# Kernel tuning notes

Measured on AMD Instinct MI355X. Metric: run time of the kernel, lower is better.

The kernel has to match this reference:

```python
import jax, jax.numpy as jnp
import numpy as np

B = 64          # graphs per batch
NN = 4096       # nodes per graph (64x64 lattice)
N = B * NN      # total nodes
DEG = 4         # avg degree
E = N * DEG     # total directed edges
DIN, H, L = 1, 128, 64


def setup_inputs() -> dict:
    key = jax.random.key(0)
    ks = jax.random.split(key, 16)
    x = jax.random.normal(ks[0], (N, DIN), dtype=jnp.float32)
    eps = jax.random.normal(ks[1], (B, L), dtype=jnp.float32)
    # per-graph random edges, offset so they never cross graphs
    src = jax.random.randint(ks[2], (E,), 0, NN)
    dst = jax.random.randint(ks[3], (E,), 0, NN)
    off = (jnp.arange(E) // (NN * DEG)) * NN
    edge_index = jnp.stack([src + off, dst + off]).astype(jnp.int32)
    batch = (jnp.arange(N) // NN).astype(jnp.int32)
    s = 0.02
    p = lambda k, shp: s * jax.random.normal(k, shp, dtype=jnp.float32)
    return {
        "x": x, "eps": eps,
        "enc_w1": p(ks[4], (DIN, H)), "enc_b1": jnp.zeros((H,), jnp.float32),
        "enc_w2": p(ks[5], (H, H)),   "enc_b2": jnp.zeros((H,), jnp.float32),
        "mu_w": p(ks[6], (H, L)),     "mu_b": jnp.zeros((L,), jnp.float32),
        "lv_w": p(ks[7], (H, L)),     "lv_b": jnp.zeros((L,), jnp.float32),
        "zn_w": p(ks[8], (L, H)),     "zn_b": jnp.zeros((H,), jnp.float32),
        "dec_w1": p(ks[9], (H, H)),   "dec_b1": jnp.zeros((H,), jnp.float32),
        "dec_w2": p(ks[10], (H, H)),  "dec_b2": jnp.zeros((H,), jnp.float32),
        "out_w": p(ks[11], (H, 1)),   "out_b": jnp.zeros((1,), jnp.float32),
        "edge_index": edge_index, "batch": batch,
    }


def _gcn(h, w, b, row, col, norm, n):
    # PyG GCNConv: xW -> gather at row, scale by sym-norm, scatter-sum at col, + bias
    hw = h @ w
    msg = hw[row] * norm[:, None]
    return jax.ops.segment_sum(msg, col, num_segments=n) + b


def reference(x, eps, enc_w1, enc_b1, enc_w2, enc_b2, mu_w, mu_b, lv_w, lv_b,
              zn_w, zn_b, dec_w1, dec_b1, dec_w2, dec_b2, out_w, out_b,
              edge_index, batch):
    n = x.shape[0]
    b = eps.shape[0]
    nn_ = n // b
    # add self-loops, symmetric GCN normalization (shared by all convs)
    loops = jnp.arange(n, dtype=edge_index.dtype)
    row = jnp.concatenate([edge_index[0], loops])
    col = jnp.concatenate([edge_index[1], loops])
    deg = jax.ops.segment_sum(jnp.ones_like(col, dtype=x.dtype), col, num_segments=n)
    dinv = jnp.where(deg > 0, jax.lax.rsqrt(deg), 0.0)
    norm = dinv[row] * dinv[col]
    h = jax.nn.relu(_gcn(x, enc_w1, enc_b1, row, col, norm, n))
    h = jax.nn.relu(_gcn(h, enc_w2, enc_b2, row, col, norm, n))
    cnt = jax.ops.segment_sum(jnp.ones((n,), x.dtype), batch, num_segments=b)
    hg = jax.ops.segment_sum(h, batch, num_segments=b) / cnt[:, None]
    mu = hg @ mu_w + mu_b
    logvar = hg @ lv_w + lv_b
    # ---- reparameterize ----
    z = mu + jnp.exp(0.5 * logvar) * eps
    zn = z @ zn_w + zn_b          # [B, H]
    hd = zn[batch]                # [N, H]
    hd = jax.nn.relu(_gcn(hd, dec_w1, dec_b1, row, col, norm, n))
    hd = jax.nn.relu(_gcn(hd, dec_w2, dec_b2, row, col, norm, n))
    spin = jnp.tanh(hd @ out_w + out_b)   # [N, 1]
    recon = spin.reshape(b, nn_)
    return (recon, mu, logvar, z)
```

## Files before the change

kernel.cpp:

```cpp
#include <hip/hip_runtime.h>
#include <math.h>

#define NTOT 262144
#define BG   64
#define NNPG 4096
#define ET   1048576
#define EPG  16384
#define EPB  4096
#define HD   128
#define LD   64
#define NSEG 129
#define TN   256
#define MCAP ET

__device__ __forceinline__ void swz(int b, int& g, int& j){
  int xcd = b & 7, q = b >> 3;
  g = (q >> 2)*8 + xcd;
  j = q & 3;
}

__device__ __forceinline__ void tab_base(
    int tid, const float* __restrict__ wsrc, const float* __restrict__ bsrc,
    const float* __restrict__ w2, float* __restrict__ tout, int* __restrict__ nfout,
    float* __restrict__ ACg,
    float* ws, float* bs, int* ks, float (*red)[128][4], int* nfsh)
{
  int k = tid & 127, qg = tid >> 7;
  if (qg == 0){
    float w = wsrc[k], b = bsrc[k];
    float t; int kind;
    if (w != 0.0f){ t = -b / w; kind = (w > 0.0f) ? 0 : 1; }
    else          { t = INFINITY; kind = 2; }
    ws[k] = w; bs[k] = b; ks[k] = kind;
    if (tout) tout[k] = t;
  }
  __syncthreads();
  if (tid == 0){
    int c = 0;
    for (int q = 0; q < 128; q++) c += (ks[q] != 2) ? 1 : 0;
    *nfsh = c;
    if (nfout) *nfout = c;
  }
  float a0=0.f, c0=0.f, an=0.f, cn=0.f;
  #pragma unroll
  for (int u = 0; u < 16; u++){
    int q = qg*16 + u;
    float v = w2[q*HD + k];
    int kd = ks[q];
    float wq = ws[q], bq = bs[q];
    bool m0 = (kd == 1) || (kd == 2 && bq > 0.f);
    bool mn = (kd == 0) || (kd == 2 && bq > 0.f);
    float wv = wq*v, bv = bq*v;
    a0 += m0 ? wv : 0.f; c0 += m0 ? bv : 0.f;
    an += mn ? wv : 0.f; cn += mn ? bv : 0.f;
  }
  red[qg][k][0]=a0; red[qg][k][1]=c0; red[qg][k][2]=an; red[qg][k][3]=cn;
  __syncthreads();
  int nf = *nfsh;
  int base = (k>>2)*8 + (k&3);
  if (qg == 0){
    float A0=0.f,C0=0.f,An=0.f,Cn=0.f;
    #pragma unroll
    for (int p = 0; p < 8; p++){
      A0+=red[p][k][0]; C0+=red[p][k][1]; An+=red[p][k][2]; Cn+=red[p][k][3];
    }
    ACg[base] = A0; ACg[base+4] = C0;
    ACg[(size_t)nf*256 + base] = An; ACg[(size_t)nf*256 + base + 4] = Cn;
  }
}

__device__ __forceinline__ void tab_extras(
    int g, int tid, const float* __restrict__ wsrc, const float* __restrict__ bsrc,
    const float* __restrict__ w2, const int* __restrict__ segUsed,
    const int* __restrict__ nfA, float* __restrict__ ACbase,
    float* ws, float* bs, float* tsh, int* ks, int* rr, float (*red)[128][4])
{
  int nf = nfA[g];
  unsigned any = 0;
  for (int wd = 0; wd < 5; wd++){
    unsigned m = (unsigned)segUsed[g*8 + wd];
    if (wd == 0) m &= ~1u;
    if ((nf >> 5) == wd) m &= ~(1u << (nf & 31));
    any |= m;
  }
  if (any == 0) return;
  int k = tid & 127, qg = tid >> 7;
  if (qg == 0){
    float w = wsrc[g*HD + k], b = bsrc[k];
    float t; int kind;
    if (w != 0.0f){ t = -b / w; kind = (w > 0.0f) ? 0 : 1; }
    else          { t = INFINITY; kind = 2; }
    ws[k] = w; bs[k] = b; tsh[k] = t; ks[k] = kind;
  }
  __syncthreads();
  if (qg == 0){
    float t = tsh[k];
    int r = 0;
    for (int q = 0; q < 128; q++){
      if (ks[q] != 2){
        float tq = tsh[q];
        if (tq < t || (tq == t && q < k)) r++;
      }
    }
    rr[k] = r;
  }
  __syncthreads();
  float* ACg = ACbase + (size_t)g*NSEG*256;
  int base = (k>>2)*8 + (k&3);
  for (int wd = 0; wd < 5; wd++){
    unsigned m = (unsigned)segUsed[g*8 + wd];
    if (wd == 0) m &= ~1u;
    if ((nf >> 5) == wd) m &= ~(1u << (nf & 31));
    while (m){
      int bit = __ffs(m) - 1;
      m &= m - 1;
      int s = wd*32 + bit;
      float pa=0.f, pc=0.f;
      #pragma unroll
      for (int u = 0; u < 16; u++){
        int q = qg*16 + u;
        int kd = ks[q];
        bool act = (kd == 0) ? (rr[q] < s) : (kd == 1) ? (rr[q] >= s) : (bs[q] > 0.f);
        float v = act ? w2[q*HD + k] : 0.f;
        pa = fmaf(ws[q], v, pa); pc = fmaf(bs[q], v, pc);
      }
      red[qg][k][0]=pa; red[qg][k][1]=pc;
      __syncthreads();
      if (qg == 0){
        float A=0.f,C=0.f;
        #pragma unroll
        for (int p = 0; p < 8; p++){ A+=red[p][k][0]; C+=red[p][k][1]; }
        ACg[(size_t)s*256 + base] = A; ACg[(size_t)s*256 + base + 4] = C;
      }
      __syncthreads();
    }
  }
}

__global__ void __launch_bounds__(1024) k_count(const int* __restrict__ ei,
                                                const float* __restrict__ w1,
                                                const float* __restrict__ b1,
                                                const float* __restrict__ w2,
                                                int* __restrict__ cntJ,
                                                float* __restrict__ t1, int* __restrict__ nfp,
                                                float* __restrict__ AC1,
                                                float* __restrict__ hgsum,
                                                int* __restrict__ mcnt,
                                                int* __restrict__ segU1,
                                                int* __restrict__ segU){
  __shared__ union {
    int h[NNPG];
    struct { float ws[128], bs[128]; int ks[128], nfsh;
             float red[8][128][4]; } t;
  } u;
  int tid = threadIdx.x;
  if (blockIdx.x == 256){
    for (int idx = tid; idx < BG*HD; idx += 1024) hgsum[idx] = 0.f;
    if (tid < 2) mcnt[tid] = 0;
    if (tid < 8) segU1[tid] = 0;
    if (tid < BG*8) segU[tid] = 0;
    tab_base(tid, w1, b1, w2, t1, nfp, AC1,
             u.t.ws, u.t.bs, u.t.ks, u.t.red, &u.t.nfsh);
    return;
  }
  int g, j; swz(blockIdx.x, g, j);
  #pragma unroll
  for (int k = tid; k < NNPG; k += 1024) u.h[k] = 0;
  __syncthreads();
  int gbase = g*NNPG;
  const int4* dsts4 = (const int4*)(ei + ET + g*EPG + j*EPB);
  int4 D = dsts4[tid];
  atomicAdd(&u.h[D.x - gbase], 1); atomicAdd(&u.h[D.y - gbase], 1);
  atomicAdd(&u.h[D.z - gbase], 1); atomicAdd(&u.h[D.w - gbase], 1);
  __syncthreads();
  int* plane = cntJ + j*NTOT + gbase;
  #pragma unroll
  for (int k = tid; k < NNPG; k += 1024) plane[k] = u.h[k];
}

__global__ void __launch_bounds__(1024) k_edge1(
    const int* __restrict__ ei, const int* __restrict__ cntJ,
    const float* __restrict__ x, float2* __restrict__ xd,
    float2* __restrict__ accJ)
{
  __shared__ float2 sxd[NNPG];
  __shared__ float ax[NNPG];
  __shared__ float s1[NNPG];
  int tid = threadIdx.x;
  int g, j; swz(blockIdx.x, g, j);
  int gbase = g*NNPG;
  const int4* srcs4 = (const int4*)(ei + g*EPG + j*EPB);
  const int4* dsts4 = (const int4*)(ei + ET + g*EPG + j*EPB);
  int4 S = srcs4[tid], D = dsts4[tid];
  {
    int i0 = 4*tid;
    int4 c0 = *(const int4*)(cntJ + 0*NTOT + gbase + i0);
    int4 c1 = *(const int4*)(cntJ + 1*NTOT + gbase + i0);
    int4 c2 = *(const int4*)(cntJ + 2*NTOT + gbase + i0);
    int4 c3 = *(const int4*)(cntJ + 3*NTOT + gbase + i0);
    float4 xv = *(const float4*)(x + gbase + i0);
    float2 p0 = make_float2(xv.x, rsqrtf((float)(c0.x+c1.x+c2.x+c3.x) + 1.0f));
    float2 p1 = make_float2(xv.y, rsqrtf((float)(c0.y+c1.y+c2.y+c3.y) + 1.0f));
    float2 p2 = make_float2(xv.z, rsqrtf((float)(c0.z+c1.z+c2.z+c3.z) + 1.0f));
    float2 p3 = make_float2(xv.w, rsqrtf((float)(c0.w+c1.w+c2.w+c3.w) + 1.0f));
    sxd[i0+0] = p0; sxd[i0+1] = p1; sxd[i0+2] = p2; sxd[i0+3] = p3;
    if (j == 0){
      float4* xd4 = (float4*)(xd + gbase);
      xd4[2*tid+0] = make_float4(p0.x, p0.y, p1.x, p1.y);
      xd4[2*tid+1] = make_float4(p2.x, p2.y, p3.x, p3.y);
    }
    *(float4*)(ax + i0) = make_float4(0.f,0.f,0.f,0.f);
    *(float4*)(s1 + i0) = make_float4(0.f,0.f,0.f,0.f);
  }
  __syncthreads();
  #define P1(s_, d_) { float2 sd = sxd[(s_) - gbase]; int dl = (d_) - gbase; \
    atomicAdd(&ax[dl], sd.y * sd.x); \
    atomicAdd(&s1[dl], sd.y); }
  P1(S.x, D.x); P1(S.y, D.y); P1(S.z, D.z); P1(S.w, D.w);
  #undef P1
  __syncthreads();
  float4* ap = (float4*)(accJ + (size_t)j*NTOT + gbase);
  ap[2*tid+0] = make_float4(ax[4*tid+0], s1[4*tid+0], ax[4*tid+1], s1[4*tid+1]);
  ap[2*tid+1] = make_float4(ax[4*tid+2], s1[4*tid+2], ax[4*tid+3], s1[4*tid+3]);
}

__global__ void k_pack(const float2* __restrict__ xd, const float2* __restrict__ accJ,
                       const float* __restrict__ t1,
                       float4* __restrict__ rec, float* __restrict__ srowA,
                       int* __restrict__ segU1){
  __shared__ float ts[128];
  __shared__ int used[8];
  int tid = threadIdx.x;
  if (tid < 128) ts[tid] = t1[tid];
  if (tid < 8) used[tid] = 0;
  __syncthreads();
  int i = blockIdx.x*256 + tid;
  float2 xdv = xd[i];
  float2 a0 = accJ[0*NTOT + i], a1 = accJ[1*NTOT + i];
  float2 a2 = accJ[2*NTOT + i], a3 = accJ[3*NTOT + i];
  float axs = (a0.x + a1.x) + (a2.x + a3.x);
  float s1s = (a0.y + a1.y) + (a2.y + a3.y);
  float di = xdv.y;
  float ax = di * (di * xdv.x + axs);
  float sr = di * (di + s1s);
  int sc = 0;
  for (int q = 0; q < 128; q++) sc += (ts[q] < ax) ? 1 : 0;
  rec[i] = make_float4(di, di*ax, di*sr, __int_as_float(sc));
  srowA[i] = sr;
  atomicOr(&used[sc>>5], 1u << (sc & 31));
  __syncthreads();
  if (tid < 8 && used[tid]) atomicOr(&segU1[tid], used[tid]);
}

__global__ void __launch_bounds__(1024) k_edge2enc(
    const int* __restrict__ ei, const float4* __restrict__ rec,
    const int* __restrict__ nfp, float4* __restrict__ sums4,
    int2* __restrict__ missL, int* __restrict__ mcnt,
    const float* __restrict__ enc_w1, const float* __restrict__ enc_b1,
    const float* __restrict__ enc_w2, const int* __restrict__ segU1,
    float* __restrict__ AC1)
{
  __shared__ union {
    float sf[NNPG*4];
    struct { float ws[128], bs[128], tsh[128];
             int ks[128], rr[128]; float red[8][128][4]; } t;
  } u;
  int tid = threadIdx.x;
  if (blockIdx.x == 256){
    tab_extras(0, tid, enc_w1, enc_b1, enc_w2, segU1, nfp, AC1,
               u.t.ws, u.t.bs, u.t.tsh, u.t.ks, u.t.rr, u.t.red);
    return;
  }
  int g, j; swz(blockIdx.x, g, j);
  int gbase = g*NNPG;
  int nf = nfp[0];
  const int4* srcs4 = (const int4*)(ei + g*EPG + j*EPB);
  const int4* dsts4 = (const int4*)(ei + ET + g*EPG + j*EPB);
  int4 S = srcs4[tid], D = dsts4[tid];
  float4 r1 = rec[S.x], r2 = rec[S.y], r3 = rec[S.z], r4 = rec[S.w];
  float4* sf4 = (float4*)u.sf;
  #pragma unroll
  for (int k = 0; k < 4; k++) sf4[tid + k*1024] = make_float4(0.f,0.f,0.f,0.f);
  __syncthreads();
  #define E1(r_, s_, d_) { int dl = (d_) - gbase; int sb = __float_as_int(r_.w); \
    atomicAdd(&u.sf[dl*4+0], r_.y); atomicAdd(&u.sf[dl*4+1], r_.x); \
    if (sb == nf) { atomicAdd(&u.sf[dl*4+2], r_.y); atomicAdd(&u.sf[dl*4+3], r_.x); } \
    else if (sb != 0) { int ix = atomicAdd(&mcnt[0], 1); \
      if (ix < MCAP) missL[ix] = make_int2(d_, s_); } }
  E1(r1, S.x, D.x); E1(r2, S.y, D.y); E1(r3, S.z, D.z); E1(r4, S.w, D.w);
  #undef E1
  __syncthreads();
  float4* sp = sums4 + (size_t)j*NTOT + gbase;
  #pragma unroll
  for (int k = 0; k < 4; k++) sp[tid + k*1024] = sf4[tid + k*1024];
}

__global__ void __launch_bounds__(256) k_enc_fin(
    const float4* __restrict__ rec, const float4* __restrict__ sums4,
    const float4* __restrict__ AC, const float* __restrict__ b2,
    const int* __restrict__ nfp, const int2* __restrict__ missL,
    const int* __restrict__ mcnt, float* __restrict__ hgsum)
{
  __shared__ float4 sS[TN];
  __shared__ float4 sRA[TN];
  __shared__ float red[256*4];
  int bid = blockIdx.x, g = bid & 63, part = bid >> 6;
  int tid = threadIdx.x, lane = tid & 31, nrow = tid >> 5;
  int base = g*NNPG + part*TN;
  int nf = nfp[0];
  {
    int i = base + tid;
    sRA[tid] = rec[i];
    float4 a = sums4[0*NTOT + i], b = sums4[1*NTOT + i];
    float4 c = sums4[2*NTOT + i], d = sums4[3*NTOT + i];
    sS[tid] = make_float4(a.x+b.x+c.x+d.x, a.y+b.y+c.y+d.y,
                          a.z+b.z+c.z+d.z, a.w+b.w+c.w+d.w);
  }
  __syncthreads();
  const float4* q0 = AC + (size_t)lane*2;
  const float4* qn = AC + ((size_t)nf*32 + lane)*2;
  float4 A0 = q0[0], C0 = q0[1], An = qn[0], Cn = qn[1];
  float4 dA = make_float4(An.x-A0.x, An.y-A0.y, An.z-A0.z, An.w-A0.w);
  float4 dC = make_float4(Cn.x-C0.x, Cn.y-C0.y, Cn.z-C0.z, Cn.w-C0.w);
  float4 bb = ((const float4*)b2)[lane];
  int mc = mcnt[0]; mc = mc < MCAP ? mc : MCAP;
  float gx=0.f, gy=0.f, gz=0.f, gw=0.f;
  for (int it = 0; it < TN/8; ++it){
    int li = it*8 + nrow;
    int i = base + li;
    float4 rA = sRA[li];
    float4 s4 = sS[li];
    float accx = fmaf(s4.x,A0.x, fmaf(s4.z,dA.x, fmaf(s4.y,C0.x, s4.w*dC.x)));
    float accy = fmaf(s4.x,A0.y, fmaf(s4.z,dA.y, fmaf(s4.y,C0.y, s4.w*dC.y)));
    float accz = fmaf(s4.x,A0.z, fmaf(s4.z,dA.z, fmaf(s4.y,C0.z, s4.w*dC.z)));
    float accw = fmaf(s4.x,A0.w, fmaf(s4.z,dA.w, fmaf(s4.y,C0.w, s4.w*dC.w)));
    if (mc > 0){
      for (int e = 0; e < mc; e++){
        int2 me = missL[e];
        if (me.x == i){
          float4 r = rec[me.y];
          int sb = __float_as_int(r.w);
          const float4* qm = AC + ((size_t)sb*32 + lane)*2;
          float4 qa = qm[0], qc = qm[1];
          accx = fmaf(r.y, qa.x-A0.x, fmaf(r.x, qc.x-C0.x, accx));
          accy = fmaf(r.y, qa.y-A0.y, fmaf(r.x, qc.y-C0.y, accy));
          accz = fmaf(r.y, qa.z-A0.z, fmaf(r.x, qc.z-C0.z, accz));
          accw = fmaf(r.y, qa.w-A0.w, fmaf(r.x, qc.w-C0.w, accw));
        }
      }
    }
    int si = __float_as_int(rA.w);
    bool m0 = (si == 0);
    float4 sa, sc;
    sa.x = m0 ? A0.x : An.x; sa.y = m0 ? A0.y : An.y; sa.z = m0 ? A0.z : An.z; sa.w = m0 ? A0.w : An.w;
    sc.x = m0 ? C0.x : Cn.x; sc.y = m0 ? C0.y : Cn.y; sc.z = m0 ? C0.z : Cn.z; sc.w = m0 ? C0.w : Cn.w;
    if (si != 0 && si != nf){
      const float4* qs = AC + ((size_t)si*32 + lane)*2;
      sa = qs[0]; sc = qs[1];
    }
    float d = rA.x, d2 = d*d, ca = rA.y*d;
    gx += fmaxf(fmaf(d, accx, fmaf(ca, sa.x, d2*sc.x)) + bb.x, 0.f);
    gy += fmaxf(fmaf(d, accy, fmaf(ca, sa.y, d2*sc.y)) + bb.y, 0.f);
    gz += fmaxf(fmaf(d, accz, fmaf(ca, sa.z, d2*sc.z)) + bb.z, 0.f);
    gw += fmaxf(fmaf(d, accw, fmaf(ca, sa.w, d2*sc.w)) + bb.w, 0.f);
  }
  __syncthreads();
  red[tid*4+0] = gx; red[tid*4+1] = gy; red[tid*4+2] = gz; red[tid*4+3] = gw;
  __syncthreads();
  if (nrow == 0){
    float tx=0.f, ty=0.f, tz=0.f, tw=0.f;
    for (int r2 = 0; r2 < 8; r2++){
      int t2 = (r2*32 + lane)*4;
      tx += red[t2]; ty += red[t2+1]; tz += red[t2+2]; tw += red[t2+3];
    }
    atomicAdd(&hgsum[g*HD + lane*4 + 0], tx);
    atomicAdd(&hgsum[g*HD + lane*4 + 1], ty);
    atomicAdd(&hgsum[g*HD + lane*4 + 2], tz);
    atomicAdd(&hgsum[g*HD + lane*4 + 3], tw);
  }
}

__global__ void __launch_bounds__(1024) k_small(
    const float* __restrict__ hgsum,
    const float* __restrict__ mu_w, const float* __restrict__ mu_b,
    const float* __restrict__ lv_w, const float* __restrict__ lv_b,
    const float* __restrict__ eps,
    const float* __restrict__ zn_w, const float* __restrict__ zn_b,
    const float* __restrict__ dec_w1, const float* __restrict__ dec_b1,
    const float* __restrict__ dec_w2,
    float* __restrict__ out_mu, float* __restrict__ out_lv, float* __restrict__ out_z,
    float* __restrict__ t2, float* __restrict__ ushG, int* __restrict__ nf2,
    float* __restrict__ AC2)
{
  __shared__ float hg[128], zsh[64], znsh[128], ush[128], bsx[128];
  __shared__ int ks[128], nfsh;
  __shared__ float red[8][128][4];
  int g = blockIdx.x, tid = threadIdx.x;
  if (tid < 128) hg[tid] = hgsum[g*HD + tid] * (1.0f/4096.0f);
  __syncthreads();
  if (tid < 64){
    int l = tid;
    float m = mu_b[l], v = lv_b[l];
    for (int k = 0; k < HD; k++){
      float hv = hg[k];
      m = fmaf(hv, mu_w[k*LD + l], m);
      v = fmaf(hv, lv_w[k*LD + l], v);
    }
    int o = g*LD + l;
    out_mu[o] = m; out_lv[o] = v;
    float zv = fmaf(expf(0.5f*v), eps[o], m);
    out_z[o] = zv; zsh[l] = zv;
  }
  __syncthreads();
  if (tid < 128){
    float acc = zn_b[tid];
    for (int l = 0; l < LD; l++) acc = fmaf(zsh[l], zn_w[l*HD + tid], acc);
    znsh[tid] = acc;
  }
  __syncthreads();
  if (tid < 128){
    float acc = 0.f;
    for (int j = 0; j < HD; j++) acc = fmaf(znsh[j], dec_w1[j*HD + tid], acc);
    ushG[g*HD + tid] = acc;
    ush[tid] = acc;
    float b = dec_b1[tid];
    bsx[tid] = b;
    float t; int kind;
    if (acc != 0.0f){ t = -b / acc; kind = (acc > 0.0f) ? 0 : 1; }
    else            { t = INFINITY; kind = 2; }
    t2[g*HD + tid] = t; ks[tid] = kind;
  }
  __syncthreads();
  if (tid == 0){
    int c = 0;
    for (int q = 0; q < 128; q++) c += (ks[q] != 2) ? 1 : 0;
    nf2[g] = c; nfsh = c;
  }
  __syncthreads();
  int k = tid & 127, qg = tid >> 7;
  float a0=0.f, c0=0.f, an=0.f, cn=0.f;
  #pragma unroll
  for (int u = 0; u < 16; u++){
    int q = qg*16 + u;
    float v = dec_w2[q*HD + k];
    int kd = ks[q];
    float wq = ush[q], bq = bsx[q];
    bool m0 = (kd == 1) || (kd == 2 && bq > 0.f);
    bool mn = (kd == 0) || (kd == 2 && bq > 0.f);
    float wv = wq*v, bv = bq*v;
    a0 += m0 ? wv : 0.f; c0 += m0 ? bv : 0.f;
    an += mn ? wv : 0.f; cn += mn ? bv : 0.f;
  }
  red[qg][k][0]=a0; red[qg][k][1]=c0; red[qg][k][2]=an; red[qg][k][3]=cn;
  __syncthreads();
  if (qg == 0){
    float A0=0.f,C0=0.f,An=0.f,Cn=0.f;
    #pragma unroll
    for (int p = 0; p < 8; p++){
      A0+=red[p][k][0]; C0+=red[p][k][1]; An+=red[p][k][2]; Cn+=red[p][k][3];
    }
    float* ACg = AC2 + (size_t)g*NSEG*256;
    int base = (k>>2)*8 + (k&3);
    int nf = nfsh;
    ACg[base] = A0; ACg[base+4] = C0;
    ACg[(size_t)nf*256 + base] = An; ACg[(size_t)nf*256 + base + 4] = Cn;
  }
}

__global__ void k_seg2(const float* __restrict__ t2, const float* __restrict__ srowA,
                       float4* __restrict__ rec, int* __restrict__ segUsed){
  __shared__ float ts[128];
  __shared__ int used[8];
  int tid = threadIdx.x;
  int i = blockIdx.x*256 + tid;
  int g = blockIdx.x >> 4;
  if (tid < 128) ts[tid] = t2[g*HD + tid];
  if (tid < 8) used[tid] = 0;
  __syncthreads();
  float a = srowA[i];
  int sc = 0;
  for (int q = 0; q < 128; q++) sc += (ts[q] < a) ? 1 : 0;
  float4 r = rec[i];
  r.y = __int_as_float(sc);
  rec[i] = r;
  atomicOr(&used[sc>>5], 1u << (sc & 31));
  __syncthreads();
  if (tid < 8 && used[tid]) atomicOr(&segUsed[g*8 + tid], used[tid]);
}

__global__ void __launch_bounds__(1024) k_edge2dec(
    const int* __restrict__ ei, const float4* __restrict__ rec,
    const int* __restrict__ nf2, float4* __restrict__ sums4,
    int2* __restrict__ missL, int* __restrict__ mcnt,
    const float* __restrict__ ushG, const float* __restrict__ dec_b1,
    const float* __restrict__ dec_w2, const int* __restrict__ segU,
    float* __restrict__ AC2)
{
  __shared__ union {
    float sf[NNPG*4];
    struct { float ws[128], bs[128], tsh[128];
             int ks[128], rr[128]; float red[8][128][4]; } t;
  } u;
  int tid = threadIdx.x;
  if (blockIdx.x >= 256){
    tab_extras(blockIdx.x - 256, tid, ushG, dec_b1, dec_w2, segU, nf2, AC2,
               u.t.ws, u.t.bs, u.t.tsh, u.t.ks, u.t.rr, u.t.red);
    return;
  }
  int g, j; swz(blockIdx.x, g, j);
  int gbase = g*NNPG;
  int nf = nf2[g];
  const int4* srcs4 = (const int4*)(ei + g*EPG + j*EPB);
  const int4* dsts4 = (const int4*)(ei + ET + g*EPG + j*EPB);
  int4 S = srcs4[tid], D = dsts4[tid];
  float4 r1 = rec[S.x], r2 = rec[S.y], r3 = rec[S.z], r4 = rec[S.w];
  float4* sf4 = (float4*)u.sf;
  #pragma unroll
  for (int k = 0; k < 4; k++) sf4[tid + k*1024] = make_float4(0.f,0.f,0.f,0.f);
  __syncthreads();
  #define E2(r_, s_, d_) { int dl = (d_) - gbase; int sb = __float_as_int(r_.y); \
    atomicAdd(&u.sf[dl*4+0], r_.z); atomicAdd(&u.sf[dl*4+1], r_.x); \
    if (sb == nf) { atomicAdd(&u.sf[dl*4+2], r_.z); atomicAdd(&u.sf[dl*4+3], r_.x); } \
    else if (sb != 0) { int ix = atomicAdd(&mcnt[1], 1); \
      if (ix < MCAP) missL[ix] = make_int2(d_, s_); } }
  E2(r1, S.x, D.x); E2(r2, S.y, D.y); E2(r3, S.z, D.z); E2(r4, S.w, D.w);
  #undef E2
  __syncthreads();
  float4* sp = sums4 + (size_t)j*NTOT + gbase;
  #pragma unroll
  for (int k = 0; k < 4; k++) sp[tid + k*1024] = sf4[tid + k*1024];
}

__global__ void __launch_bounds__(256) k_dec_fin(
    const float4* __restrict__ rec, const float4* __restrict__ sums4,
    const float4* __restrict__ AC2, const float* __restrict__ b2,
    const float* __restrict__ ow, const float* __restrict__ ob,
    const int* __restrict__ nf2, const int2* __restrict__ missL,
    const int* __restrict__ mcnt, float* __restrict__ recon)
{
  __shared__ float4 sS[TN];
  __shared__ float4 sRA[TN];
  int bid = blockIdx.x, g = bid & 63, part = bid >> 6;
  int tid = threadIdx.x, lane = tid & 31, nrow = tid >> 5;
  int base = g*NNPG + part*TN;
  int nf = nf2[g];
  const float4* AC = AC2 + (size_t)g*NSEG*64;
  {
    int i = base + tid;
    sRA[tid] = rec[i];
    float4 a = sums4[0*NTOT + i], b = sums4[1*NTOT + i];
    float4 c = sums4[2*NTOT + i], d = sums4[3*NTOT + i];
    sS[tid] = make_float4(a.x+b.x+c.x+d.x, a.y+b.y+c.y+d.y,
                          a.z+b.z+c.z+d.z, a.w+b.w+c.w+d.w);
  }
  __syncthreads();
  const float4* q0 = AC + (size_t)lane*2;
  const float4* qn = AC + ((size_t)nf*32 + lane)*2;
  float4 A0 = q0[0], C0 = q0[1], An = qn[0], Cn = qn[1];
  float4 dA = make_float4(An.x-A0.x, An.y-A0.y, An.z-A0.z, An.w-A0.w);
  float4 dC = make_float4(Cn.x-C0.x, Cn.y-C0.y, Cn.z-C0.z, Cn.w-C0.w);
  float4 bb  = ((const float4*)b2)[lane];
  float4 owv = ((const float4*)ow)[lane];
  float obv = ob[0];
  int mc = mcnt[1]; mc = mc < MCAP ? mc : MCAP;
  for (int it = 0; it < TN/8; ++it){
    int li = it*8 + nrow;
    int i = base + li;
    float4 rA = sRA[li];
    float4 s4 = sS[li];
    float accx = fmaf(s4.x,A0.x, fmaf(s4.z,dA.x, fmaf(s4.y,C0.x, s4.w*dC.x)));
    float accy = fmaf(s4.x,A0.y, fmaf(s4.z,dA.y, fmaf(s4.y,C0.y, s4.w*dC.y)));
    float accz = fmaf(s4.x,A0.z, fmaf(s4.z,dA.z, fmaf(s4.y,C0.z, s4.w*dC.z)));
    float accw = fmaf(s4.x,A0.w, fmaf(s4.z,dA.w, fmaf(s4.y,C0.w, s4.w*dC.w)));
    if (mc > 0){
      for (int e = 0; e < mc; e++){
        int2 me = missL[e];
        if (me.x == i){
          float4 r = rec[me.y];
          int sb = __float_as_int(r.y);
          const float4* qm = AC + ((size_t)sb*32 + lane)*2;
          float4 qa = qm[0], qc = qm[1];
          accx = fmaf(r.z, qa.x-A0.x, fmaf(r.x, qc.x-C0.x, accx));
          accy = fmaf(r.z, qa.y-A0.y, fmaf(r.x, qc.y-C0.y, accy));
          accz = fmaf(r.z, qa.z-A0.z, fmaf(r.x, qc.z-C0.z, accz));
          accw = fmaf(r.z, qa.w-A0.w, fmaf(r.x, qc.w-C0.w, accw));
        }
      }
    }
    int si = __float_as_int(rA.y);
    bool m0 = (si == 0);
    float4 sa, sc;
    sa.x = m0 ? A0.x : An.x; sa.y = m0 ? A0.y : An.y; sa.z = m0 ? A0.z : An.z; sa.w = m0 ? A0.w : An.w;
    sc.x = m0 ? C0.x : Cn.x; sc.y = m0 ? C0.y : Cn.y; sc.z = m0 ? C0.z : Cn.z; sc.w = m0 ? C0.w : Cn.w;
    if (si != 0 && si != nf){
      const float4* qs = AC + ((size_t)si*32 + lane)*2;
      sa = qs[0]; sc = qs[1];
    }
    float d = rA.x, d2 = d*d, ca = rA.z*d;
    float hx = fmaxf(fmaf(d, accx, fmaf(ca, sa.x, d2*sc.x)) + bb.x, 0.f);
    float hy = fmaxf(fmaf(d, accy, fmaf(ca, sa.y, d2*sc.y)) + bb.y, 0.f);
    float hz = fmaxf(fmaf(d, accz, fmaf(ca, sa.z, d2*sc.z)) + bb.z, 0.f);
    float hw = fmaxf(fmaf(d, accw, fmaf(ca, sa.w, d2*sc.w)) + bb.w, 0.f);
    float dsum = hx*owv.x + hy*owv.y + hz*owv.z + hw*owv.w;
    for (int o2 = 16; o2 > 0; o2 >>= 1) dsum += __shfl_down(dsum, o2, 32);
    if (lane == 0) recon[i] = tanhf(dsum + obv);
  }
}

extern "C" void kernel_launch(void* const* d_in, const int* in_sizes, int n_in,
                              void* d_out, int out_size, void* d_ws, size_t ws_size,
                              hipStream_t stream){
  (void)in_sizes; (void)n_in; (void)out_size; (void)ws_size;
  const float* x      = (const float*)d_in[0];
  const float* eps    = (const float*)d_in[1];
  const float* enc_w1 = (const float*)d_in[2];
  const float* enc_b1 = (const float*)d_in[3];
  const float* enc_w2 = (const float*)d_in[4];
  const float* enc_b2 = (const float*)d_in[5];
  const float* mu_w   = (const float*)d_in[6];
  const float* mu_b   = (const float*)d_in[7];
  const float* lv_w   = (const float*)d_in[8];
  const float* lv_b   = (const float*)d_in[9];
  const float* zn_w   = (const float*)d_in[10];
  const float* zn_b   = (const float*)d_in[11];
  const float* dec_w1 = (const float*)d_in[12];
  const float* dec_b1 = (const float*)d_in[13];
  const float* dec_w2 = (const float*)d_in[14];
  const float* dec_b2 = (const float*)d_in[15];
  const float* out_w  = (const float*)d_in[16];
  const float* out_b  = (const float*)d_in[17];
  const int*   ei     = (const int*)d_in[18];

  float* out       = (float*)d_out;
  float* out_recon = out;
  float* out_mu    = out + NTOT;
  float* out_lv    = out_mu + BG*LD;
  float* out_z     = out_lv + BG*LD;

  char* w = (char*)d_ws;
  size_t off_b = 0;
  auto alloc = [&](size_t bytes)->void*{
    void* p = w + off_b;
    off_b += (bytes + 255) & ~(size_t)255;
    return p;
  };
  char*   regA   = (char*) alloc((size_t)4*NTOT*16);
  int*    cntJ   = (int*)   regA;
  float2* accJ   = (float2*)(regA + (size_t)4*NTOT*4);
  float4* sums4  = (float4*)regA;
  float2* xd     = (float2*)alloc((size_t)NTOT*8);
  float4* rec    = (float4*)alloc((size_t)NTOT*16);
  float*  srowA  = (float*) alloc((size_t)NTOT*4);
  int2*   missL  = (int2*)  alloc((size_t)MCAP*8);
  float*  t1     = (float*) alloc(128*4);
  int*    nf1    = (int*)   alloc(256);
  int*    nf2    = (int*)   alloc(BG*4);
  int*    segU1  = (int*)   alloc(8*4);
  int*    segU   = (int*)   alloc(BG*8*4);
  float*  t2     = (float*) alloc((size_t)BG*HD*4);
  float*  ushG   = (float*) alloc((size_t)BG*HD*4);
  float*  AC1    = (float*) alloc((size_t)NSEG*256*4);
  float*  AC2    = (float*) alloc((size_t)BG*NSEG*256*4);
  float*  hgsum  = (float*) alloc((size_t)BG*HD*4);
  int*    mcnt   = (int*)   alloc(256);


  k_count <<<257, 1024, 0, stream>>>(ei, enc_w1, enc_b1, enc_w2, cntJ, t1, nf1,
                                     AC1, hgsum, mcnt, segU1, segU);
  k_edge1 <<<256, 1024, 0, stream>>>(ei, cntJ, x, xd, accJ);
  k_pack  <<<NTOT/256, 256, 0, stream>>>(xd, accJ, t1, rec, srowA, segU1);

  k_edge2enc<<<257, 1024, 0, stream>>>(ei, rec, nf1, sums4, missL, mcnt,
                                       enc_w1, enc_b1, enc_w2, segU1, AC1);
  k_enc_fin <<<1024, 256, 0, stream>>>(rec, sums4, (const float4*)AC1, enc_b2,
                                       nf1, missL, mcnt, hgsum);

  k_small<<<BG, 1024, 0, stream>>>(hgsum, mu_w, mu_b, lv_w, lv_b, eps,
                                   zn_w, zn_b, dec_w1, dec_b1, dec_w2,
                                   out_mu, out_lv, out_z, t2, ushG, nf2, AC2);

  k_seg2<<<NTOT/256, 256, 0, stream>>>(t2, srowA, rec, segU);

  k_edge2dec<<<320, 1024, 0, stream>>>(ei, rec, nf2, sums4, missL, mcnt,
                                       ushG, dec_b1, dec_w2, segU, AC2);
  k_dec_fin <<<1024, 256, 0, stream>>>(rec, sums4, (const float4*)AC2, dec_b2,
                                       out_w, out_b, nf2, missL, mcnt, out_recon);
}
```

Measured before the change: 150.0 us.

## Fuse decoder segment-index computation into edge and finalize kernels, drop k_seg2

```diff
diff --git a/kernel.cpp b/kernel.cpp
--- a/kernel.cpp
+++ b/kernel.cpp
@@ -70,15 +70,14 @@
 }
 
 __device__ __forceinline__ void tab_extras(
-    int g, int tid, const float* __restrict__ wsrc, const float* __restrict__ bsrc,
-    const float* __restrict__ w2, const int* __restrict__ segUsed,
-    const int* __restrict__ nfA, float* __restrict__ ACbase,
+    int tid, const float* __restrict__ wsrcRow, const float* __restrict__ bsrc,
+    const float* __restrict__ w2, const int* segBits, int nf,
+    float* __restrict__ ACg,
     float* ws, float* bs, float* tsh, int* ks, int* rr, float (*red)[128][4])
 {
-  int nf = nfA[g];
   unsigned any = 0;
   for (int wd = 0; wd < 5; wd++){
-    unsigned m = (unsigned)segUsed[g*8 + wd];
+    unsigned m = (unsigned)segBits[wd];
     if (wd == 0) m &= ~1u;
     if ((nf >> 5) == wd) m &= ~(1u << (nf & 31));
     any |= m;
@@ -86,7 +85,7 @@
   if (any == 0) return;
   int k = tid & 127, qg = tid >> 7;
   if (qg == 0){
-    float w = wsrc[g*HD + k], b = bsrc[k];
+    float w = wsrcRow[k], b = bsrc[k];
     float t; int kind;
     if (w != 0.0f){ t = -b / w; kind = (w > 0.0f) ? 0 : 1; }
     else          { t = INFINITY; kind = 2; }
@@ -105,10 +104,9 @@
     rr[k] = r;
   }
   __syncthreads();
-  float* ACg = ACbase + (size_t)g*NSEG*256;
   int base = (k>>2)*8 + (k&3);
   for (int wd = 0; wd < 5; wd++){
-    unsigned m = (unsigned)segUsed[g*8 + wd];
+    unsigned m = (unsigned)segBits[wd];
     if (wd == 0) m &= ~1u;
     if ((nf >> 5) == wd) m &= ~(1u << (nf & 31));
     while (m){
@@ -146,8 +144,7 @@
                                                 float* __restrict__ AC1,
                                                 float* __restrict__ hgsum,
                                                 int* __restrict__ mcnt,
-                                                int* __restrict__ segU1,
-                                                int* __restrict__ segU){
+                                                int* __restrict__ segU1){
   __shared__ union {
     int h[NNPG];
     struct { float ws[128], bs[128]; int ks[128], nfsh;
@@ -158,7 +155,6 @@
     for (int idx = tid; idx < BG*HD; idx += 1024) hgsum[idx] = 0.f;
     if (tid < 2) mcnt[tid] = 0;
     if (tid < 8) segU1[tid] = 0;
-    if (tid < BG*8) segU[tid] = 0;
     tab_base(tid, w1, b1, w2, t1, nfp, AC1,
              u.t.ws, u.t.bs, u.t.ks, u.t.red, &u.t.nfsh);
     return;
@@ -267,7 +263,7 @@
   } u;
   int tid = threadIdx.x;
   if (blockIdx.x == 256){
-    tab_extras(0, tid, enc_w1, enc_b1, enc_w2, segU1, nfp, AC1,
+    tab_extras(tid, enc_w1, enc_b1, enc_w2, segU1, nfp[0], AC1,
                u.t.ws, u.t.bs, u.t.tsh, u.t.ks, u.t.rr, u.t.red);
     return;
   }
@@ -467,43 +463,36 @@
   }
 }
 
-__global__ void k_seg2(const float* __restrict__ t2, const float* __restrict__ srowA,
-                       float4* __restrict__ rec, int* __restrict__ segUsed){
-  __shared__ float ts[128];
-  __shared__ int used[8];
-  int tid = threadIdx.x;
-  int i = blockIdx.x*256 + tid;
-  int g = blockIdx.x >> 4;
-  if (tid < 128) ts[tid] = t2[g*HD + tid];
-  if (tid < 8) used[tid] = 0;
-  __syncthreads();
-  float a = srowA[i];
-  int sc = 0;
-  for (int q = 0; q < 128; q++) sc += (ts[q] < a) ? 1 : 0;
-  float4 r = rec[i];
-  r.y = __int_as_float(sc);
-  rec[i] = r;
-  atomicOr(&used[sc>>5], 1u << (sc & 31));
-  __syncthreads();
-  if (tid < 8 && used[tid]) atomicOr(&segUsed[g*8 + tid], used[tid]);
-}
-
 __global__ void __launch_bounds__(1024) k_edge2dec(
     const int* __restrict__ ei, const float4* __restrict__ rec,
+    const float* __restrict__ srowA, const float* __restrict__ t2,
     const int* __restrict__ nf2, float4* __restrict__ sums4,
     int2* __restrict__ missL, int* __restrict__ mcnt,
     const float* __restrict__ ushG, const float* __restrict__ dec_b1,
-    const float* __restrict__ dec_w2, const int* __restrict__ segU,
-    float* __restrict__ AC2)
+    const float* __restrict__ dec_w2, float* __restrict__ AC2)
 {
   __shared__ union {
     float sf[NNPG*4];
     struct { float ws[128], bs[128], tsh[128];
-             int ks[128], rr[128]; float red[8][128][4]; } t;
+             int ks[128], rr[128]; float red[8][128][4]; int used[8]; } t;
   } u;
+  __shared__ unsigned short sSeg[NNPG];
+  __shared__ float tscan[128];
   int tid = threadIdx.x;
   if (blockIdx.x >= 256){
-    tab_extras(blockIdx.x - 256, tid, ushG, dec_b1, dec_w2, segU, nf2, AC2,
+    int g = blockIdx.x - 256;
+    if (tid < 128) tscan[tid] = t2[g*HD + tid];
+    if (tid < 8) u.t.used[tid] = 0;
+    __syncthreads();
+    for (int n = tid; n < NNPG; n += 1024){
+      float a = srowA[g*NNPG + n];
+      int sc = 0;
+      for (int q = 0; q < 128; q++) sc += (tscan[q] < a) ? 1 : 0;
+      atomicOr(&u.t.used[sc>>5], 1u << (sc & 31));
+    }
+    __syncthreads();
+    tab_extras(tid, ushG + g*HD, dec_b1, dec_w2, u.t.used, nf2[g],
+               AC2 + (size_t)g*NSEG*256,
                u.t.ws, u.t.bs, u.t.tsh, u.t.ks, u.t.rr, u.t.red);
     return;
   }
@@ -514,11 +503,19 @@
   const int4* dsts4 = (const int4*)(ei + ET + g*EPG + j*EPB);
   int4 S = srcs4[tid], D = dsts4[tid];
   float4 r1 = rec[S.x], r2 = rec[S.y], r3 = rec[S.z], r4 = rec[S.w];
+  if (tid < 128) tscan[tid] = t2[g*HD + tid];
   float4* sf4 = (float4*)u.sf;
   #pragma unroll
   for (int k = 0; k < 4; k++) sf4[tid + k*1024] = make_float4(0.f,0.f,0.f,0.f);
   __syncthreads();
-  #define E2(r_, s_, d_) { int dl = (d_) - gbase; int sb = __float_as_int(r_.y); \
+  for (int n = tid; n < NNPG; n += 1024){
+    float a = srowA[gbase + n];
+    int sc = 0;
+    for (int q = 0; q < 128; q++) sc += (tscan[q] < a) ? 1 : 0;
+    sSeg[n] = (unsigned short)sc;
+  }
+  __syncthreads();
+  #define E2(r_, s_, d_) { int dl = (d_) - gbase; int sb = (int)sSeg[(s_) - gbase]; \
     atomicAdd(&u.sf[dl*4+0], r_.z); atomicAdd(&u.sf[dl*4+1], r_.x); \
     if (sb == nf) { atomicAdd(&u.sf[dl*4+2], r_.z); atomicAdd(&u.sf[dl*4+3], r_.x); } \
     else if (sb != 0) { int ix = atomicAdd(&mcnt[1], 1); \
@@ -533,6 +530,7 @@
 
 __global__ void __launch_bounds__(256) k_dec_fin(
     const float4* __restrict__ rec, const float4* __restrict__ sums4,
+    const float* __restrict__ srowA, const float* __restrict__ t2,
     const float4* __restrict__ AC2, const float* __restrict__ b2,
     const float* __restrict__ ow, const float* __restrict__ ob,
     const int* __restrict__ nf2, const int2* __restrict__ missL,
@@ -540,11 +538,14 @@
 {
   __shared__ float4 sS[TN];
   __shared__ float4 sRA[TN];
+  __shared__ float ts[128];
+  __shared__ int sSi[TN];
   int bid = blockIdx.x, g = bid & 63, part = bid >> 6;
   int tid = threadIdx.x, lane = tid & 31, nrow = tid >> 5;
   int base = g*NNPG + part*TN;
   int nf = nf2[g];
   const float4* AC = AC2 + (size_t)g*NSEG*64;
+  if (tid < 128) ts[tid] = t2[g*HD + tid];
   {
     int i = base + tid;
     sRA[tid] = rec[i];
@@ -552,6 +553,13 @@
     float4 c = sums4[2*NTOT + i], d = sums4[3*NTOT + i];
     sS[tid] = make_float4(a.x+b.x+c.x+d.x, a.y+b.y+c.y+d.y,
                           a.z+b.z+c.z+d.z, a.w+b.w+c.w+d.w);
+  }
+  __syncthreads();
+  {
+    float a = srowA[base + tid];
+    int sc = 0;
+    for (int q = 0; q < 128; q++) sc += (ts[q] < a) ? 1 : 0;
+    sSi[tid] = sc;
   }
   __syncthreads();
   const float4* q0 = AC + (size_t)lane*2;
@@ -577,7 +585,9 @@
         int2 me = missL[e];
         if (me.x == i){
           float4 r = rec[me.y];
-          int sb = __float_as_int(r.y);
+          float am = srowA[me.y];
+          int sb = 0;
+          for (int q = 0; q < 128; q++) sb += (ts[q] < am) ? 1 : 0;
           const float4* qm = AC + ((size_t)sb*32 + lane)*2;
           float4 qa = qm[0], qc = qm[1];
           accx = fmaf(r.z, qa.x-A0.x, fmaf(r.x, qc.x-C0.x, accx));
@@ -587,7 +597,7 @@
         }
       }
     }
-    int si = __float_as_int(rA.y);
+    int si = sSi[li];
     bool m0 = (si == 0);
     float4 sa, sc;
     sa.x = m0 ? A0.x : An.x; sa.y = m0 ? A0.y : An.y; sa.z = m0 ? A0.z : An.z; sa.w = m0 ? A0.w : An.w;
@@ -656,7 +666,6 @@
   int*    nf1    = (int*)   alloc(256);
   int*    nf2    = (int*)   alloc(BG*4);
   int*    segU1  = (int*)   alloc(8*4);
-  int*    segU   = (int*)   alloc(BG*8*4);
   float*  t2     = (float*) alloc((size_t)BG*HD*4);
   float*  ushG   = (float*) alloc((size_t)BG*HD*4);
   float*  AC1    = (float*) alloc((size_t)NSEG*256*4);
@@ -666,7 +675,7 @@
 
 
   k_count <<<257, 1024, 0, stream>>>(ei, enc_w1, enc_b1, enc_w2, cntJ, t1, nf1,
-                                     AC1, hgsum, mcnt, segU1, segU);
+                                     AC1, hgsum, mcnt, segU1);
   k_edge1 <<<256, 1024, 0, stream>>>(ei, cntJ, x, xd, accJ);
   k_pack  <<<NTOT/256, 256, 0, stream>>>(xd, accJ, t1, rec, srowA, segU1);
 
@@ -679,10 +688,9 @@
                                    zn_w, zn_b, dec_w1, dec_b1, dec_w2,
                                    out_mu, out_lv, out_z, t2, ushG, nf2, AC2);
 
-  k_seg2<<<NTOT/256, 256, 0, stream>>>(t2, srowA, rec, segU);
-
-  k_edge2dec<<<320, 1024, 0, stream>>>(ei, rec, nf2, sums4, missL, mcnt,
-                                       ushG, dec_b1, dec_w2, segU, AC2);
-  k_dec_fin <<<1024, 256, 0, stream>>>(rec, sums4, (const float4*)AC2, dec_b2,
+  k_edge2dec<<<320, 1024, 0, stream>>>(ei, rec, srowA, t2, nf2, sums4, missL,
+                                       mcnt, ushG, dec_b1, dec_w2, AC2);
+  k_dec_fin <<<1024, 256, 0, stream>>>(rec, sums4, srowA, t2,
+                                       (const float4*)AC2, dec_b2,
                                        out_w, out_b, nf2, missL, mcnt, out_recon);
 }
```

After: 176.2 us. 1.17x slower.
